# Kernel optimization log

Hardware: AMD Instinct MI355X
Metric: run time of the kernel (lower is better)

Reference implementation:

```python
import jax, jax.numpy as jnp
import numpy as np

N_NODES = 50000


def gcn_conv(x, edge_index, edge_weight, W, b):
    """PyG GCNConv: x' = D^{-1/2}(A+I)D^{-1/2} (x W) + b, with edge weights."""
    n = x.shape[0]
    x = x @ W  # transform first (PyG order): [N, d_out]
    row, col = edge_index[0], edge_index[1]  # source -> target
    # add self loops with weight 1
    loop = jnp.arange(n)
    row = jnp.concatenate([row, loop])
    col = jnp.concatenate([col, loop])
    ew = jnp.concatenate([edge_weight, jnp.ones((n,), dtype=x.dtype)])
    # symmetric normalization based on (weighted) in-degree at targets
    deg = jax.ops.segment_sum(ew, col, num_segments=n)
    dis = jnp.where(deg > 0, jax.lax.rsqrt(deg), 0.0)
    norm = dis[row] * ew * dis[col]  # [E+N]
    # gather-scale-scatter aggregation
    msg = x[row] * norm[:, None]  # [E+N, d_out]
    out = jax.ops.segment_sum(msg, col, num_segments=n)
    return out + b


def setup_inputs() -> dict:
    key = jax.random.key(0)
    ks = jax.random.split(key, 9)
    E = 800000
    bert_output = jax.random.normal(ks[0], (N_NODES, 1024), dtype=jnp.float32)
    edge_index = jax.random.randint(ks[1], (2, E), 0, N_NODES, dtype=jnp.int64)
    edge_weight = jax.random.uniform(ks[2], (E,), dtype=jnp.float32)
    s1 = 1.0 / np.sqrt(1024)
    s2 = 1.0 / np.sqrt(512)
    s3 = 1.0 / np.sqrt(128)
    W1 = jax.random.uniform(ks[3], (1024, 512), jnp.float32, -s1, s1)
    b1 = jnp.zeros((512,), jnp.float32)
    W2 = jax.random.uniform(ks[4], (512, 128), jnp.float32, -s2, s2)
    b2 = jnp.zeros((128,), jnp.float32)
    Wfc = jax.random.uniform(ks[5], (128, 14), jnp.float32, -s3, s3)
    bfc = jax.random.uniform(ks[6], (14,), jnp.float32, -s3, s3)
    return {
        "bert_output": bert_output,
        "edge_index": edge_index,
        "edge_weight": edge_weight,
        "W1": W1, "b1": b1, "W2": W2, "b2": b2, "Wfc": Wfc, "bfc": bfc,
    }


def reference(bert_output, edge_index, edge_weight, W1, b1, W2, b2, Wfc, bfc):
    h = jax.nn.relu(gcn_conv(bert_output, edge_index, edge_weight, W1, b1))
    h = jax.nn.relu(gcn_conv(h, edge_index, edge_weight, W2, b2))
    logits = h @ Wfc + bfc
    return jax.nn.sigmoid(logits)
```

## Files before the change

### kernel.cpp

```cpp
#include <hip/hip_runtime.h>
#include <stdint.h>

__device__ __forceinline__ float bf2f(unsigned short h) {
  union { uint32_t u; float f; } v; v.u = ((uint32_t)h) << 16; return v.f;
}
__device__ __forceinline__ unsigned short f2bf(float f) {
  union { float f; uint32_t u; } v; v.f = f;
  uint32_t u = v.u;
  u += 0x7FFFu + ((u >> 16) & 1u);
  return (unsigned short)(u >> 16);
}
__device__ __forceinline__ uint32_t pack2bf(float a, float b) {
  return (uint32_t)f2bf(a) | ((uint32_t)f2bf(b) << 16);
}
__device__ __forceinline__ int ld_idx(const void* p, size_t i, int is64) {
  return is64 ? (int)((const long long*)p)[i] : ((const int*)p)[i];
}
__device__ __forceinline__ float ld_w(const void* p, size_t i, int f32) {
  return f32 ? ((const float*)p)[i] : bf2f(((const unsigned short*)p)[i]);
}

typedef __attribute__((ext_vector_type(8))) short short8;
typedef __attribute__((ext_vector_type(4))) float floatx4;

__device__ __forceinline__ void gl2lds16(const unsigned short* g, unsigned short* l) {
  __builtin_amdgcn_global_load_lds(
      (const __attribute__((address_space(1))) uint32_t*)(const void*)g,
      (__attribute__((address_space(3))) uint32_t*)(void*)l,
      16, 0, 0);
}

__global__ void bgcn_init_probe(float* __restrict__ deg, int* __restrict__ counts,
                                int* __restrict__ fill, int n,
                                const uint32_t* __restrict__ xw,
                                const uint32_t* __restrict__ iw,
                                int* __restrict__ flags) {
  int i = blockIdx.x * 256 + threadIdx.x;
  if (i < n) { deg[i] = 1.0f; counts[i] = 0; fill[i] = 0; }
  if (blockIdx.x == 0 && threadIdx.x < 64) {
    int lane = threadIdx.x;
    int hits = 0;
    #pragma unroll
    for (int j = 0; j < 4; ++j) {
      uint32_t b = (xw[lane * 4 + j] >> 8) & 0x7F;
      hits += (b >= 0x38 && b <= 0x41) ? 1 : 0;
    }
    #pragma unroll
    for (int off = 32; off; off >>= 1) hits += __shfl_xor(hits, off);
    unsigned long long nz = __ballot(iw[2 * lane + 1] != 0u);
    if (lane == 0) {
      flags[0] = (hits < 128) ? 1 : 0;
      flags[1] = (nz == 0ull) ? 1 : 0;
    }
  }
}

__global__ void bgcn_cvt8(const void* __restrict__ src, unsigned short* __restrict__ dst,
                          int n8, const int* __restrict__ flags) {
  int i = blockIdx.x * 256 + threadIdx.x;
  if (i >= n8) return;
  size_t o = (size_t)i * 8;
  uint4 d;
  if (flags[0]) {
    const float4* f = (const float4*)((const float*)src + o);
    float4 f0 = f[0], f1 = f[1];
    d = make_uint4(pack2bf(f0.x, f0.y), pack2bf(f0.z, f0.w),
                   pack2bf(f1.x, f1.y), pack2bf(f1.z, f1.w));
  } else {
    d = *(const uint4*)((const unsigned short*)src + o);
  }
  *(uint4*)(dst + o) = d;
}
__global__ __launch_bounds__(256) void bgcn_cvt_t(
    const void* __restrict__ src, unsigned short* __restrict__ dst,
    int K, int N, const int* __restrict__ flags) {
  __shared__ unsigned short tile[32][33];
  int k0 = blockIdx.x * 32, n0 = blockIdx.y * 32;
  int tx = threadIdx.x & 31, ty = threadIdx.x >> 5;
  bool f32 = flags[0];
  #pragma unroll
  for (int i = 0; i < 4; ++i) {
    size_t s = (size_t)(k0 + ty + i * 8) * N + n0 + tx;
    tile[ty + i * 8][tx] = f32 ? f2bf(((const float*)src)[s])
                               : ((const unsigned short*)src)[s];
  }
  __syncthreads();
  #pragma unroll
  for (int i = 0; i < 4; ++i)
    dst[(size_t)(n0 + ty + i * 8) * K + k0 + tx] = tile[tx][ty + i * 8];
}
__global__ void bgcn_cvt_small(const void* b1, const void* b2,
                               const void* wfc, const void* bfc,
                               unsigned short* db1, unsigned short* db2,
                               unsigned short* dwfc, unsigned short* dbfc,
                               const int* __restrict__ flags) {
  int i = blockIdx.x * 256 + threadIdx.x;
  bool f32 = flags[0];
  const void* s; unsigned short* d; int j;
  if (i < 512)            { s = b1;  d = db1;  j = i; }
  else if (i < 640)       { s = b2;  d = db2;  j = i - 512; }
  else if (i < 2432)      { s = wfc; d = dwfc; j = i - 640; }
  else if (i < 2446)      { s = bfc; d = dbfc; j = i - 2432; }
  else return;
  d[j] = f32 ? f2bf(((const float*)s)[j]) : ((const unsigned short*)s)[j];
}

__global__ void bgcn_deg_hist(const void* __restrict__ ei, const void* __restrict__ ew,
                              const int* __restrict__ flags,
                              float* __restrict__ deg, int* __restrict__ counts, int E) {
  int e = blockIdx.x * 256 + threadIdx.x;
  if (e >= E) return;
  int c = ld_idx(ei, (size_t)E + e, flags[1]);
  atomicAdd(&deg[c], ld_w(ew, e, flags[0]));
  atomicAdd(&counts[c], 1);
}
__global__ void bgcn_scan_block(const int* __restrict__ counts, int* __restrict__ rowptr,
                                int* __restrict__ blocksum,
                                const float* __restrict__ deg, float* __restrict__ dis,
                                int n) {
  __shared__ int buf[1024];
  int gid = blockIdx.x * 1024 + threadIdx.x;
  int v = (gid < n) ? counts[gid] : 0;
  buf[threadIdx.x] = v;
  __syncthreads();
  for (int off = 1; off < 1024; off <<= 1) {
    int x = (threadIdx.x >= off) ? buf[threadIdx.x - off] : 0;
    __syncthreads();
    buf[threadIdx.x] += x;
    __syncthreads();
  }
  if (gid < n) {
    rowptr[gid + 1] = buf[threadIdx.x];
    dis[gid] = rsqrtf(deg[gid]);
  }
  if (threadIdx.x == 1023) blocksum[blockIdx.x] = buf[1023];
}
__global__ void bgcn_scan_tops(int* __restrict__ blocksum, int nb) {
  __shared__ int buf[1024];
  int t = threadIdx.x;
  int v = (t < nb) ? blocksum[t] : 0;
  buf[t] = v;
  __syncthreads();
  for (int off = 1; off < 1024; off <<= 1) {
    int x = (t >= off) ? buf[t - off] : 0;
    __syncthreads();
    buf[t] += x;
    __syncthreads();
  }
  if (t < nb) blocksum[t] = buf[t] - v;
}
__global__ void bgcn_scan_add(int* __restrict__ rowptr, const int* __restrict__ blocksum, int n) {
  int gid = blockIdx.x * 1024 + threadIdx.x;
  if (gid < n) rowptr[gid + 1] += blocksum[blockIdx.x];
  if (gid == 0) rowptr[0] = 0;
}
__global__ void bgcn_scatter(const void* __restrict__ ei, const void* __restrict__ ew,
                             const int* __restrict__ flags,
                             const float* __restrict__ dis,
                             const int* __restrict__ rowptr, int* __restrict__ fill,
                             int* __restrict__ esrc, float* __restrict__ enorm, int E) {
  int e = blockIdx.x * 256 + threadIdx.x;
  if (e >= E) return;
  int is64 = flags[1];
  int r = ld_idx(ei, e, is64), c = ld_idx(ei, (size_t)E + e, is64);
  int pos = rowptr[c] + atomicAdd(&fill[c], 1);
  esrc[pos]  = r;
  enorm[pos] = dis[r] * ld_w(ew, e, flags[0]) * dis[c];
}

__global__ __launch_bounds__(256) void bgcn_gemm_lds(
    const unsigned short* __restrict__ A,
    const unsigned short* __restrict__ Bt,
    unsigned short* __restrict__ C,
    int M, int N, int K, int nblk_bits, int wpx, int nwork) {
  __shared__ unsigned short Abuf[128 * 32];
  __shared__ unsigned short Bbuf[128 * 32];
  int t = threadIdx.x;
  int wave = t >> 6, lane = t & 63;
  int xcd = blockIdx.x & 7;
  int g   = blockIdx.x >> 3;
  int work = xcd * wpx + g;
  if (work >= nwork) return;
  int nblk = work & ((1 << nblk_bits) - 1);
  int mblk = work >> nblk_bits;
  int m0 = mblk * 128, n0 = nblk * 128;

  floatx4 acc[4][4];
  #pragma unroll
  for (int i = 0; i < 4; ++i)
    #pragma unroll
    for (int j = 0; j < 4; ++j)
      #pragma unroll
      for (int r = 0; r < 4; ++r) acc[i][j][r] = 0.0f;

  int rii  = lane >> 2;
  int koff = (lane & 3) * 8;
  int ar0 = m0 + wave * 32 + rii;      if (ar0 >= M) ar0 = M - 1;
  int ar1 = m0 + wave * 32 + 16 + rii; if (ar1 >= M) ar1 = M - 1;
  const unsigned short* Ag0 = A + (size_t)ar0 * K + koff;
  const unsigned short* Ag1 = A + (size_t)ar1 * K + koff;
  const unsigned short* Bg0 = Bt + (size_t)(n0 + wave * 32 + rii) * K + koff;
  const unsigned short* Bg1 = Bg0 + (size_t)16 * K;
  unsigned short* Al0 = Abuf + (wave * 32) * 32 + lane * 8;
  unsigned short* Al1 = Abuf + (wave * 32 + 16) * 32 + lane * 8;
  unsigned short* Bl0 = Bbuf + (wave * 32) * 32 + lane * 8;
  unsigned short* Bl1 = Bbuf + (wave * 32 + 16) * 32 + lane * 8;

  int fr = lane & 15;
  int fk = (lane >> 4) * 8;
  int mw = (wave & 1) * 64;
  int nw = (wave >> 1) * 64;

  for (int k0 = 0; k0 < K; k0 += 32) {
    gl2lds16(Ag0 + k0, Al0);
    gl2lds16(Ag1 + k0, Al1);
    gl2lds16(Bg0 + k0, Bl0);
    gl2lds16(Bg1 + k0, Bl1);
    __syncthreads();

    short8 afr[4], bfr[4];
    #pragma unroll
    for (int i = 0; i < 4; ++i)
      afr[i] = *(const short8*)(Abuf + (mw + i * 16 + fr) * 32 + fk);
    #pragma unroll
    for (int i = 0; i < 4; ++i)
      bfr[i] = *(const short8*)(Bbuf + (nw + i * 16 + fr) * 32 + fk);
    #pragma unroll
    for (int mt = 0; mt < 4; ++mt)
      #pragma unroll
      for (int nt = 0; nt < 4; ++nt)
        acc[mt][nt] = __builtin_amdgcn_mfma_f32_16x16x32_bf16(afr[mt], bfr[nt], acc[mt][nt], 0, 0, 0);
    __syncthreads();
  }

  int col_l = lane & 15;
  int row_b = (lane >> 4) * 4;
  #pragma unroll
  for (int mt = 0; mt < 4; ++mt)
    #pragma unroll
    for (int nt = 0; nt < 4; ++nt)
      #pragma unroll
      for (int r = 0; r < 4; ++r) {
        int m = m0 + mw + mt * 16 + row_b + r;
        if (m < M)
          C[(size_t)m * N + n0 + nw + nt * 16 + col_l] = f2bf(acc[mt][nt][r]);
      }
}

#define GST 40
__global__ __launch_bounds__(256, 2) void bgcn_gemm128(
    const void* __restrict__ Araw, int a_probe, const int* __restrict__ flags,
    const unsigned short* __restrict__ Bt,
    unsigned short* __restrict__ C,
    int M, int N, int K, int nblk_bits) {
  __shared__ unsigned short Abuf[128 * GST];
  __shared__ unsigned short Bbuf[128 * GST];
  const bool a_fp32 = a_probe && flags[0];
  int t = threadIdx.x;
  int wave = t >> 6, lane = t & 63;
  int bx = blockIdx.x;
  int nblk = bx & ((1 << nblk_bits) - 1);
  int mblk = bx >> nblk_bits;
  int m0 = mblk * 128, n0 = nblk * 128;

  floatx4 acc[4][4];
  #pragma unroll
  for (int i = 0; i < 4; ++i)
    #pragma unroll
    for (int j = 0; j < 4; ++j)
      #pragma unroll
      for (int r = 0; r < 4; ++r) acc[i][j][r] = 0.0f;

  int srow  = t >> 1;
  int skoff = (t & 1) * 16;
  int am = m0 + srow; if (am >= M) am = M - 1;
  const float*          Af = (const float*)Araw          + (size_t)am * K + skoff;
  const unsigned short* Ah = (const unsigned short*)Araw + (size_t)am * K + skoff;
  const unsigned short* Bp = Bt + (size_t)(n0 + srow) * K + skoff;
  unsigned short* AL = Abuf + srow * GST + skoff;
  unsigned short* BL = Bbuf + srow * GST + skoff;

  int fr = lane & 15;
  int fk = (lane >> 4) * 8;
  int mw = (wave & 1) * 64;
  int nw = (wave >> 1) * 64;

  for (int k0 = 0; k0 < K; k0 += 32) {
    uint4 a0, a1;
    if (a_fp32) {
      float4 f0 = *(const float4*)(Af + k0);
      float4 f1 = *(const float4*)(Af + k0 + 4);
      float4 f2 = *(const float4*)(Af + k0 + 8);
      float4 f3 = *(const float4*)(Af + k0 + 12);
      a0 = make_uint4(pack2bf(f0.x, f0.y), pack2bf(f0.z, f0.w),
                      pack2bf(f1.x, f1.y), pack2bf(f1.z, f1.w));
      a1 = make_uint4(pack2bf(f2.x, f2.y), pack2bf(f2.z, f2.w),
                      pack2bf(f3.x, f3.y), pack2bf(f3.z, f3.w));
    } else {
      a0 = *(const uint4*)(Ah + k0);
      a1 = *(const uint4*)(Ah + k0 + 8);
    }
    uint4 b0 = *(const uint4*)(Bp + k0);
    uint4 b1 = *(const uint4*)(Bp + k0 + 8);
    *(uint4*)AL       = a0;
    *(uint4*)(AL + 8) = a1;
    *(uint4*)BL       = b0;
    *(uint4*)(BL + 8) = b1;
    __syncthreads();

    short8 afr[4], bfr[4];
    #pragma unroll
    for (int i = 0; i < 4; ++i)
      afr[i] = *(const short8*)(Abuf + (mw + i * 16 + fr) * GST + fk);
    #pragma unroll
    for (int i = 0; i < 4; ++i)
      bfr[i] = *(const short8*)(Bbuf + (nw + i * 16 + fr) * GST + fk);
    #pragma unroll
    for (int mt = 0; mt < 4; ++mt)
      #pragma unroll
      for (int nt = 0; nt < 4; ++nt)
        acc[mt][nt] = __builtin_amdgcn_mfma_f32_16x16x32_bf16(afr[mt], bfr[nt], acc[mt][nt], 0, 0, 0);
    __syncthreads();
  }

  int col_l = lane & 15;
  int row_b = (lane >> 4) * 4;
  #pragma unroll
  for (int mt = 0; mt < 4; ++mt)
    #pragma unroll
    for (int nt = 0; nt < 4; ++nt)
      #pragma unroll
      for (int r = 0; r < 4; ++r) {
        int m = m0 + mw + mt * 16 + row_b + r;
        if (m < M)
          C[(size_t)m * N + n0 + nw + nt * 16 + col_l] = f2bf(acc[mt][nt][r]);
      }
}

__device__ __forceinline__ void accum4(float* acc, uint2 r, float w) {
  acc[0] += w * bf2f((unsigned short)(r.x & 0xffff));
  acc[1] += w * bf2f((unsigned short)(r.x >> 16));
  acc[2] += w * bf2f((unsigned short)(r.y & 0xffff));
  acc[3] += w * bf2f((unsigned short)(r.y >> 16));
}
__device__ __forceinline__ void accum2(float* acc, uint32_t r, float w) {
  acc[0] += w * bf2f((unsigned short)(r & 0xffff));
  acc[1] += w * bf2f((unsigned short)(r >> 16));
}

template <int F, int WPN, bool FUSE_FC>
__global__ __launch_bounds__(256) void bgcn_aggregate(
    const unsigned short* __restrict__ H,
    const int* __restrict__ rowptr,
    const int* __restrict__ esrc,
    const float* __restrict__ enorm,
    const float* __restrict__ dis,
    const unsigned short* __restrict__ bias,
    unsigned short* __restrict__ Out,
    const unsigned short* __restrict__ Wfc,
    const unsigned short* __restrict__ bfc,
    float* __restrict__ fcout,
    int n_nodes) {
  constexpr int FPW = F / WPN;
  constexpr int VPL = FPW / 64;
  constexpr int NPB = 4 / WPN;
  constexpr int DEPTH = 16;

  int t = threadIdx.x;
  int lane = t & 63;
  int wid = __builtin_amdgcn_readfirstlane(t >> 6);
  int c = blockIdx.x * NPB + wid / WPN;
  if (c >= n_nodes) return;
  c = __builtin_amdgcn_readfirstlane(c);
  int h = wid % WPN;

  int beg = __builtin_amdgcn_readfirstlane(rowptr[c]);
  int end = __builtin_amdgcn_readfirstlane(rowptr[c + 1]);
  float ds = dis[c];

  int fo = h * FPW + lane * VPL;
  const unsigned short* Hl = H + fo;

  uint2 rs;
  union { uint2 v; unsigned short u[4]; } bu;
  if constexpr (VPL == 4) {
    rs = *(const uint2*)(Hl + (size_t)c * F);
    bu.v = *(const uint2*)(bias + fo);
  } else {
    rs.x = *(const uint32_t*)(Hl + (size_t)c * F);
    bu.v.x = *(const uint32_t*)(bias + fo);
  }

  float acc[VPL];
  #pragma unroll
  for (int j = 0; j < VPL; ++j) acc[j] = 0.0f;

  for (int base = beg; base < end; base += 64) {
    int n = end - base;
    if (n > 64) n = 64;
    n = __builtin_amdgcn_readfirstlane(n);
    int   sv = 0;
    float wv = 0.0f;
    if (lane < n) {
      sv = esrc[base + lane];
      wv = enorm[base + lane];
    }
    for (int q0 = 0; q0 < n; q0 += DEPTH) {
      uint2 r[DEPTH];
      float w[DEPTH];
      #pragma unroll
      for (int j = 0; j < DEPTH; ++j) {
        int q = q0 + j;
        int qs = (q < n) ? q : 0;
        int sq = __builtin_amdgcn_readlane(sv, qs);
        w[j] = __int_as_float(
            __builtin_amdgcn_readlane(__float_as_int(wv), q));
        const unsigned short* src = Hl + (size_t)sq * F;
        if constexpr (VPL == 4) r[j] = *(const uint2*)src;
        else                    r[j].x = *(const uint32_t*)src;
      }
      #pragma unroll
      for (int j = 0; j < DEPTH; ++j) {
        if constexpr (VPL == 4) accum4(acc, r[j], w[j]);
        else                    accum2(acc, r[j].x, w[j]);
      }
    }
  }

  float wself = ds * ds;
  if constexpr (VPL == 4) accum4(acc, rs, wself);
  else                    accum2(acc, rs.x, wself);

  float vpost[VPL];
  #pragma unroll
  for (int j = 0; j < VPL; ++j)
    vpost[j] = fmaxf(acc[j] + bf2f(bu.u[j]), 0.0f);

  if constexpr (FUSE_FC) {
    float part[14];
    const unsigned short* w0 = Wfc + (size_t)(2 * lane) * 14;
    #pragma unroll
    for (int o = 0; o < 14; ++o)
      part[o] = vpost[0] * bf2f(w0[o]) + vpost[1] * bf2f(w0[14 + o]);
    #pragma unroll
    for (int off = 32; off; off >>= 1)
      #pragma unroll
      for (int o = 0; o < 14; ++o)
        part[o] += __shfl_xor(part[o], off);
    if (lane == 0) {
      float* op = fcout + (size_t)c * 14;
      #pragma unroll
      for (int o = 0; o < 14; ++o)
        op[o] = 1.0f / (1.0f + __expf(-(part[o] + bf2f(bfc[o]))));
    }
  } else {
    unsigned short ob[VPL];
    #pragma unroll
    for (int j = 0; j < VPL; ++j) ob[j] = f2bf(vpost[j]);
    if constexpr (VPL == 4) {
      uint2 st;
      st.x = (uint32_t)ob[0] | ((uint32_t)ob[1] << 16);
      st.y = (uint32_t)ob[2] | ((uint32_t)ob[3] << 16);
      *(uint2*)(Out + (size_t)c * F + fo) = st;
    } else {
      *(uint32_t*)(Out + (size_t)c * F + fo) =
          (uint32_t)ob[0] | ((uint32_t)ob[1] << 16);
    }
  }
}

static inline size_t padsz(size_t x) { return (x + 255) & ~(size_t)255; }
static inline void* wsa(char*& p, size_t bytes) {
  void* r = p;
  p += padsz(bytes);
  return r;
}

extern "C" void kernel_launch(void* const* d_in, const int* in_sizes, int n_in,
                              void* d_out, int out_size, void* d_ws, size_t ws_size,
                              hipStream_t stream) {
  const void* Xr   = d_in[0];
  const void* EIr  = d_in[1];
  const void* EWr  = d_in[2];
  const void* W1r  = d_in[3];
  const void* b1r  = d_in[4];
  const void* W2r  = d_in[5];
  const void* b2r  = d_in[6];
  const void* Wfcr = d_in[7];
  const void* bfcr = d_in[8];
  float* out = (float*)d_out;

  const int N = in_sizes[0] / 1024;
  const int E = in_sizes[2];

  size_t need = padsz((size_t)N * 512 * 2)
              + padsz((size_t)N * 1024 * 2)
              + 4 * padsz((size_t)N * 4)
              + padsz((size_t)(N + 1) * 4)
              + padsz(256 * 4)
              + 2 * padsz((size_t)E * 4)
              + padsz(1024 * 512 * 2) + padsz(512 * 128 * 2)
              + padsz(512 * 2) + padsz(128 * 2) + padsz(128 * 14 * 2)
              + padsz(32) + padsz(8);
  const bool big = ws_size >= need;

  char* p = (char*)d_ws;
  unsigned short* R1  = (unsigned short*)wsa(p, (size_t)N * 512 * 2);
  unsigned short* R2  = (unsigned short*)wsa(p, (size_t)N * (big ? 1024 : 512) * 2);
  float* deg      = (float*)wsa(p, (size_t)N * 4);
  float* dis      = (float*)wsa(p, (size_t)N * 4);
  int*   counts   = (int*)wsa(p, (size_t)N * 4);
  int*   fill     = (int*)wsa(p, (size_t)N * 4);
  int*   rowptr   = (int*)wsa(p, (size_t)(N + 1) * 4);
  int*   blocksum = (int*)wsa(p, 256 * 4);
  int*   esrc     = (int*)wsa(p, (size_t)E * 4);
  float* enorm    = (float*)wsa(p, (size_t)E * 4);
  unsigned short* W1t  = (unsigned short*)wsa(p, (size_t)1024 * 512 * 2);
  unsigned short* W2t  = (unsigned short*)wsa(p, (size_t)512 * 128 * 2);
  unsigned short* b1c  = (unsigned short*)wsa(p, 512 * 2);
  unsigned short* b2c  = (unsigned short*)wsa(p, 128 * 2);
  unsigned short* Wfcc = (unsigned short*)wsa(p, 128 * 14 * 2);
  unsigned short* bfcc = (unsigned short*)wsa(p, 32);
  int* flags      = (int*)wsa(p, 8);

  unsigned short* H1  = R1;
  unsigned short* Xbf = R2;
  unsigned short* X2  = R2;
  unsigned short* H2  = R1;

  int gN = (N + 255) / 256;
  int gE = (E + 255) / 256;

  bgcn_init_probe<<<gN, 256, 0, stream>>>(deg, counts, fill, N,
                                          (const uint32_t*)Xr, (const uint32_t*)EIr, flags);
  { dim3 g(1024 / 32, 512 / 32); bgcn_cvt_t<<<g, 256, 0, stream>>>(W1r, W1t, 1024, 512, flags); }
  { dim3 g(512 / 32, 128 / 32);  bgcn_cvt_t<<<g, 256, 0, stream>>>(W2r, W2t, 512, 128, flags); }
  bgcn_cvt_small<<<10, 256, 0, stream>>>(b1r, b2r, Wfcr, bfcr, b1c, b2c, Wfcc, bfcc, flags);
  if (big) {
    int n8 = N * 1024 / 8;
    bgcn_cvt8<<<(n8 + 255) / 256, 256, 0, stream>>>(Xr, Xbf, n8, flags);
  }

  bgcn_deg_hist<<<gE, 256, 0, stream>>>(EIr, EWr, flags, deg, counts, E);
  int nb = (N + 1023) / 1024;
  bgcn_scan_block<<<nb, 1024, 0, stream>>>(counts, rowptr, blocksum, deg, dis, N);
  bgcn_scan_tops<<<1, 1024, 0, stream>>>(blocksum, nb);
  bgcn_scan_add<<<nb, 1024, 0, stream>>>(rowptr, blocksum, N);
  bgcn_scatter<<<gE, 256, 0, stream>>>(EIr, EWr, flags, dis, rowptr, fill, esrc, enorm, E);

  int mblks = (N + 127) / 128;

  int nwork1 = mblks << 2;
  int wpx1 = (nwork1 + 7) / 8;
  wpx1 = ((wpx1 + 3) / 4) * 4;
  int nwork2 = mblks;
  int wpx2 = (nwork2 + 7) / 8;

  if (big)
    bgcn_gemm_lds<<<8 * wpx1, 256, 0, stream>>>(Xbf, W1t, H1, N, 512, 1024, 2, wpx1, nwork1);
  else
    bgcn_gemm128<<<mblks * 4, 256, 0, stream>>>(Xr, 1, flags, W1t, H1, N, 512, 1024, 2);
  bgcn_aggregate<512, 2, false><<<(N + 1) / 2, 256, 0, stream>>>(
      H1, rowptr, esrc, enorm, dis, b1c, X2, nullptr, nullptr, nullptr, N);

  bgcn_gemm_lds<<<8 * wpx2, 256, 0, stream>>>(X2, W2t, H2, N, 128, 512, 0, wpx2, nwork2);
  bgcn_aggregate<128, 1, true><<<(N + 3) / 4, 256, 0, stream>>>(
      H2, rowptr, esrc, enorm, dis, b2c, nullptr, Wfcc, bfcc, out, N);
}
```

Before: 744.1 us.

## Pack edge src/norm pairs, merge weight conversions, drop XCD remap, stage FC weights in LDS

```diff
diff --git a/kernel.cpp b/kernel.cpp
--- a/kernel.cpp
+++ b/kernel.cpp
@@ -71,13 +71,11 @@
   }
   *(uint4*)(dst + o) = d;
 }
-__global__ __launch_bounds__(256) void bgcn_cvt_t(
-    const void* __restrict__ src, unsigned short* __restrict__ dst,
-    int K, int N, const int* __restrict__ flags) {
-  __shared__ unsigned short tile[32][33];
-  int k0 = blockIdx.x * 32, n0 = blockIdx.y * 32;
+
+__device__ __forceinline__ void cvt_t_tile(const void* src, unsigned short* dst,
+                                           int K, int N, int k0, int n0, bool f32,
+                                           unsigned short (*tile)[33]) {
   int tx = threadIdx.x & 31, ty = threadIdx.x >> 5;
-  bool f32 = flags[0];
   #pragma unroll
   for (int i = 0; i < 4; ++i) {
     size_t s = (size_t)(k0 + ty + i * 8) * N + n0 + tx;
@@ -89,20 +87,31 @@
   for (int i = 0; i < 4; ++i)
     dst[(size_t)(n0 + ty + i * 8) * K + k0 + tx] = tile[tx][ty + i * 8];
 }
-__global__ void bgcn_cvt_small(const void* b1, const void* b2,
-                               const void* wfc, const void* bfc,
-                               unsigned short* db1, unsigned short* db2,
-                               unsigned short* dwfc, unsigned short* dbfc,
-                               const int* __restrict__ flags) {
-  int i = blockIdx.x * 256 + threadIdx.x;
+__global__ __launch_bounds__(256) void bgcn_cvt_weights(
+    const void* __restrict__ w1, const void* __restrict__ w2,
+    const void* b1, const void* b2, const void* wfc, const void* bfc,
+    unsigned short* __restrict__ W1t, unsigned short* __restrict__ W2t,
+    unsigned short* db1, unsigned short* db2,
+    unsigned short* dwfc, unsigned short* dbfc,
+    const int* __restrict__ flags) {
+  __shared__ unsigned short tile[32][33];
   bool f32 = flags[0];
-  const void* s; unsigned short* d; int j;
-  if (i < 512)            { s = b1;  d = db1;  j = i; }
-  else if (i < 640)       { s = b2;  d = db2;  j = i - 512; }
-  else if (i < 2432)      { s = wfc; d = dwfc; j = i - 640; }
-  else if (i < 2446)      { s = bfc; d = dbfc; j = i - 2432; }
-  else return;
-  d[j] = f32 ? f2bf(((const float*)s)[j]) : ((const unsigned short*)s)[j];
+  int b = blockIdx.x;
+  if (b < 512) {
+    cvt_t_tile(w1, W1t, 1024, 512, (b >> 4) * 32, (b & 15) * 32, f32, tile);
+  } else if (b < 576) {
+    int b2i = b - 512;
+    cvt_t_tile(w2, W2t, 512, 128, (b2i >> 2) * 32, (b2i & 3) * 32, f32, tile);
+  } else {
+    int i = (b - 576) * 256 + threadIdx.x;
+    const void* s; unsigned short* d; int j;
+    if (i < 512)            { s = b1;  d = db1;  j = i; }
+    else if (i < 640)       { s = b2;  d = db2;  j = i - 512; }
+    else if (i < 2432)      { s = wfc; d = dwfc; j = i - 640; }
+    else if (i < 2446)      { s = bfc; d = dbfc; j = i - 2432; }
+    else return;
+    d[j] = f32 ? f2bf(((const float*)s)[j]) : ((const unsigned short*)s)[j];
+  }
 }
 
 __global__ void bgcn_deg_hist(const void* __restrict__ ei, const void* __restrict__ ew,
@@ -158,31 +167,28 @@
                              const int* __restrict__ flags,
                              const float* __restrict__ dis,
                              const int* __restrict__ rowptr, int* __restrict__ fill,
-                             int* __restrict__ esrc, float* __restrict__ enorm, int E) {
+                             int2* __restrict__ epair, int E) {
   int e = blockIdx.x * 256 + threadIdx.x;
   if (e >= E) return;
   int is64 = flags[1];
   int r = ld_idx(ei, e, is64), c = ld_idx(ei, (size_t)E + e, is64);
   int pos = rowptr[c] + atomicAdd(&fill[c], 1);
-  esrc[pos]  = r;
-  enorm[pos] = dis[r] * ld_w(ew, e, flags[0]) * dis[c];
+  float nrm = dis[r] * ld_w(ew, e, flags[0]) * dis[c];
+  epair[pos] = make_int2(r, __float_as_int(nrm));
 }
 
 __global__ __launch_bounds__(256) void bgcn_gemm_lds(
     const unsigned short* __restrict__ A,
     const unsigned short* __restrict__ Bt,
     unsigned short* __restrict__ C,
-    int M, int N, int K, int nblk_bits, int wpx, int nwork) {
+    int M, int N, int K, int nblk_bits) {
   __shared__ unsigned short Abuf[128 * 32];
   __shared__ unsigned short Bbuf[128 * 32];
   int t = threadIdx.x;
   int wave = t >> 6, lane = t & 63;
-  int xcd = blockIdx.x & 7;
-  int g   = blockIdx.x >> 3;
-  int work = xcd * wpx + g;
-  if (work >= nwork) return;
-  int nblk = work & ((1 << nblk_bits) - 1);
-  int mblk = work >> nblk_bits;
+  int bx = blockIdx.x;
+  int nblk = bx & ((1 << nblk_bits) - 1);
+  int mblk = bx >> nblk_bits;
   int m0 = mblk * 128, n0 = nblk * 128;
 
   floatx4 acc[4][4];
@@ -352,8 +358,7 @@
 __global__ __launch_bounds__(256) void bgcn_aggregate(
     const unsigned short* __restrict__ H,
     const int* __restrict__ rowptr,
-    const int* __restrict__ esrc,
-    const float* __restrict__ enorm,
+    const int2* __restrict__ epair,
     const float* __restrict__ dis,
     const unsigned short* __restrict__ bias,
     unsigned short* __restrict__ Out,
@@ -364,7 +369,18 @@
   constexpr int FPW = F / WPN;
   constexpr int VPL = FPW / 64;
   constexpr int NPB = 4 / WPN;
-  constexpr int DEPTH = 16;
+  constexpr int DEPTH = 8;
+
+  __shared__ float Ws[FUSE_FC ? 14 * 128 : 1];
+  __shared__ float bs[FUSE_FC ? 16 : 1];
+  if constexpr (FUSE_FC) {
+    for (int i = threadIdx.x; i < 14 * 128; i += 256) {
+      int k = i / 14, o = i % 14;
+      Ws[o * 128 + k] = bf2f(Wfc[i]);
+    }
+    if (threadIdx.x < 14) bs[threadIdx.x] = bf2f(bfc[threadIdx.x]);
+    __syncthreads();
+  }
 
   int t = threadIdx.x;
   int lane = t & 63;
@@ -399,12 +415,8 @@
     int n = end - base;
     if (n > 64) n = 64;
     n = __builtin_amdgcn_readfirstlane(n);
-    int   sv = 0;
-    float wv = 0.0f;
-    if (lane < n) {
-      sv = esrc[base + lane];
-      wv = enorm[base + lane];
-    }
+    int2 mv = make_int2(0, 0);
+    if (lane < n) mv = epair[base + lane];
     for (int q0 = 0; q0 < n; q0 += DEPTH) {
       uint2 r[DEPTH];
       float w[DEPTH];
@@ -412,9 +424,9 @@
       for (int j = 0; j < DEPTH; ++j) {
         int q = q0 + j;
         int qs = (q < n) ? q : 0;
-        int sq = __builtin_amdgcn_readlane(sv, qs);
+        int sq = __builtin_amdgcn_readlane(mv.x, qs);
         w[j] = __int_as_float(
-            __builtin_amdgcn_readlane(__float_as_int(wv), q));
+            __builtin_amdgcn_readlane(mv.y, q));
         const unsigned short* src = Hl + (size_t)sq * F;
         if constexpr (VPL == 4) r[j] = *(const uint2*)src;
         else                    r[j].x = *(const uint32_t*)src;
@@ -437,11 +449,13 @@
     vpost[j] = fmaxf(acc[j] + bf2f(bu.u[j]), 0.0f);
 
   if constexpr (FUSE_FC) {
+    const float2* W2p = (const float2*)Ws;
     float part[14];
-    const unsigned short* w0 = Wfc + (size_t)(2 * lane) * 14;
-    #pragma unroll
-    for (int o = 0; o < 14; ++o)
-      part[o] = vpost[0] * bf2f(w0[o]) + vpost[1] * bf2f(w0[14 + o]);
+    #pragma unroll
+    for (int o = 0; o < 14; ++o) {
+      float2 wv = W2p[o * 64 + lane];
+      part[o] = vpost[0] * wv.x + vpost[1] * wv.y;
+    }
     #pragma unroll
     for (int off = 32; off; off >>= 1)
       #pragma unroll
@@ -451,7 +465,7 @@
       float* op = fcout + (size_t)c * 14;
       #pragma unroll
       for (int o = 0; o < 14; ++o)
-        op[o] = 1.0f / (1.0f + __expf(-(part[o] + bf2f(bfc[o]))));
+        op[o] = 1.0f / (1.0f + __expf(-(part[o] + bs[o])));
     }
   } else {
     unsigned short ob[VPL];
@@ -498,7 +512,7 @@
               + 4 * padsz((size_t)N * 4)
               + padsz((size_t)(N + 1) * 4)
               + padsz(256 * 4)
-              + 2 * padsz((size_t)E * 4)
+              + padsz((size_t)E * 8)
               + padsz(1024 * 512 * 2) + padsz(512 * 128 * 2)
               + padsz(512 * 2) + padsz(128 * 2) + padsz(128 * 14 * 2)
               + padsz(32) + padsz(8);
@@ -513,8 +527,7 @@
   int*   fill     = (int*)wsa(p, (size_t)N * 4);
   int*   rowptr   = (int*)wsa(p, (size_t)(N + 1) * 4);
   int*   blocksum = (int*)wsa(p, 256 * 4);
-  int*   esrc     = (int*)wsa(p, (size_t)E * 4);
-  float* enorm    = (float*)wsa(p, (size_t)E * 4);
+  int2*  epair    = (int2*)wsa(p, (size_t)E * 8);
   unsigned short* W1t  = (unsigned short*)wsa(p, (size_t)1024 * 512 * 2);
   unsigned short* W2t  = (unsigned short*)wsa(p, (size_t)512 * 128 * 2);
   unsigned short* b1c  = (unsigned short*)wsa(p, 512 * 2);
@@ -533,9 +546,8 @@
 
   bgcn_init_probe<<<gN, 256, 0, stream>>>(deg, counts, fill, N,
                                           (const uint32_t*)Xr, (const uint32_t*)EIr, flags);
-  { dim3 g(1024 / 32, 512 / 32); bgcn_cvt_t<<<g, 256, 0, stream>>>(W1r, W1t, 1024, 512, flags); }
-  { dim3 g(512 / 32, 128 / 32);  bgcn_cvt_t<<<g, 256, 0, stream>>>(W2r, W2t, 512, 128, flags); }
-  bgcn_cvt_small<<<10, 256, 0, stream>>>(b1r, b2r, Wfcr, bfcr, b1c, b2c, Wfcc, bfcc, flags);
+  bgcn_cvt_weights<<<586, 256, 0, stream>>>(W1r, W2r, b1r, b2r, Wfcr, bfcr,
+                                            W1t, W2t, b1c, b2c, Wfcc, bfcc, flags);
   if (big) {
     int n8 = N * 1024 / 8;
     bgcn_cvt8<<<(n8 + 255) / 256, 256, 0, stream>>>(Xr, Xbf, n8, flags);
@@ -546,24 +558,18 @@
   bgcn_scan_block<<<nb, 1024, 0, stream>>>(counts, rowptr, blocksum, deg, dis, N);
   bgcn_scan_tops<<<1, 1024, 0, stream>>>(blocksum, nb);
   bgcn_scan_add<<<nb, 1024, 0, stream>>>(rowptr, blocksum, N);
-  bgcn_scatter<<<gE, 256, 0, stream>>>(EIr, EWr, flags, dis, rowptr, fill, esrc, enorm, E);
+  bgcn_scatter<<<gE, 256, 0, stream>>>(EIr, EWr, flags, dis, rowptr, fill, epair, E);
 
   int mblks = (N + 127) / 128;
 
-  int nwork1 = mblks << 2;
-  int wpx1 = (nwork1 + 7) / 8;
-  wpx1 = ((wpx1 + 3) / 4) * 4;
-  int nwork2 = mblks;
-  int wpx2 = (nwork2 + 7) / 8;
-
   if (big)
-    bgcn_gemm_lds<<<8 * wpx1, 256, 0, stream>>>(Xbf, W1t, H1, N, 512, 1024, 2, wpx1, nwork1);
+    bgcn_gemm_lds<<<mblks * 4, 256, 0, stream>>>(Xbf, W1t, H1, N, 512, 1024, 2);
   else
     bgcn_gemm128<<<mblks * 4, 256, 0, stream>>>(Xr, 1, flags, W1t, H1, N, 512, 1024, 2);
   bgcn_aggregate<512, 2, false><<<(N + 1) / 2, 256, 0, stream>>>(
-      H1, rowptr, esrc, enorm, dis, b1c, X2, nullptr, nullptr, nullptr, N);
-
-  bgcn_gemm_lds<<<8 * wpx2, 256, 0, stream>>>(X2, W2t, H2, N, 128, 512, 0, wpx2, nwork2);
+      H1, rowptr, epair, dis, b1c, X2, nullptr, nullptr, nullptr, N);
+
+  bgcn_gemm_lds<<<mblks, 256, 0, stream>>>(X2, W2t, H2, N, 128, 512, 0);
   bgcn_aggregate<128, 1, true><<<(N + 3) / 4, 256, 0, stream>>>(
-      H2, rowptr, esrc, enorm, dis, b2c, nullptr, Wfcc, bfcc, out, N);
-}
+      H2, rowptr, epair, dis, b2c, nullptr, Wfcc, bfcc, out, N);
+}
```

Measured after the change: 738.0 us. Within noise of the previous version (-0.8%).
